# Kernel tuning notes

Hardware: AMD Instinct MI355X
Metric: run time of the kernel (lower is better)

Reference implementation:

```python
import jax, jax.numpy as jnp
import numpy as np


def setup_inputs() -> dict:
    key = jax.random.key(0)
    ks = jax.random.split(key, 6)
    B, C, H, W, K = 4, 64, 352, 1216, 3
    OC = K * K - 1  # 8 guide channels from convbn
    return {
        "feature": jax.random.normal(ks[0], (B, C, H, W), jnp.float32),
        "conv_w": jax.random.normal(ks[1], (OC, C, 3, 3), jnp.float32) * 0.05,
        "gamma": jax.random.uniform(ks[2], (OC,), jnp.float32, 0.5, 1.5),
        "beta": jax.random.normal(ks[3], (OC,), jnp.float32) * 0.1,
        "mean": jax.random.normal(ks[4], (OC,), jnp.float32) * 0.1,
        "var": jax.random.uniform(ks[5], (OC,), jnp.float32, 0.5, 1.5),
        "kernel_size": K,
    }


def reference(feature, conv_w, gamma, beta, mean, var, kernel_size):
    k = kernel_size
    eps = 1e-5
    # conv 3x3, stride 1, pad 1, no bias  -> [B, k*k-1, H, W]
    x = jax.lax.conv_general_dilated(
        feature, conv_w, window_strides=(1, 1), padding=((1, 1), (1, 1)),
        dimension_numbers=("NCHW", "OIHW", "NCHW"))
    c = lambda v: v[None, :, None, None]
    # BatchNorm2d in eval mode (running stats + affine)
    guide = (x - c(mean)) * (c(gamma) * jax.lax.rsqrt(c(var) + eps)) + c(beta)
    # L1-normalize across channels, middle weight = 1 - sum of the others
    gsum = jnp.sum(jnp.abs(guide), axis=1, keepdims=True)
    guide = guide / gsum
    guide_mid = 1.0 - jnp.sum(guide, axis=1, keepdims=True)
    mid = (k * k - 1) // 2
    # per-offset zero-pad each single channel into [H+k-1, W+k-1] canvas
    pads = []
    for t in range(k * k):  # fixed small loop over kernel offsets (k*k = 9)
        i, j = t // k, t % k  # top=i, bottom=k-1-i, left=j, right=k-1-j
        if t < mid:
            ch = guide[:, t:t + 1]
        elif t > mid:
            ch = guide[:, t - 1:t]
        else:
            ch = guide_mid
        pads.append(jnp.pad(ch, ((0, 0), (0, 0), (i, k - 1 - i), (j, k - 1 - j))))
    return jnp.concatenate(pads, axis=1)  # [B, k*k, H+k-1, W+k-1]
```

## Files before the change

kernel.cpp:

```cpp
#include <hip/hip_runtime.h>
#include <hip/hip_bf16.h>

#define BATCH 4
#define CIN 64
#define HH 352
#define WW 1216
#define OCH 8
#define OHH 354
#define OWW 1218
#define HW (HH * WW)

#define BH 16
#define BW 32
#define FR 18
#define FC 34
#define NPOS (FR * FC)
#define NTHR 256

typedef short bf16x8 __attribute__((ext_vector_type(8)));
typedef float f32x4  __attribute__((ext_vector_type(4)));

static __device__ __forceinline__ unsigned f2bf(float x) {
    unsigned u = __float_as_uint(x);
    return (u + 0x7FFFu + ((u >> 16) & 1u)) >> 16;
}

__global__ void repack_kernel(const float* __restrict__ conv_w,
                              const float* __restrict__ gamma,
                              const float* __restrict__ beta,
                              const float* __restrict__ mean,
                              const float* __restrict__ var,
                              unsigned short* __restrict__ wB,
                              float* __restrict__ bias)
{
    int tid = blockIdx.x * 256 + threadIdx.x;
    if (tid < 18 * 64) {
        int tc = tid >> 6;
        int lane = tid & 63;
        int tap = tc >> 1, cc = tc & 1;
        int oc = lane & 15, hi = lane >> 4;
        unsigned v[8];
#pragma unroll
        for (int j = 0; j < 8; ++j) {
            float w = 0.f;
            if (oc < 8) {
                int c = cc * 32 + hi * 8 + j;
                float scl = gamma[oc] * rsqrtf(var[oc] + 1e-5f);
                w = conv_w[((size_t)oc * CIN + c) * 9 + tap] * scl;
            }
            v[j] = f2bf(w);
        }
        uint4 pk;
        pk.x = v[0] | (v[1] << 16);
        pk.y = v[2] | (v[3] << 16);
        pk.z = v[4] | (v[5] << 16);
        pk.w = v[6] | (v[7] << 16);
        ((uint4*)wB)[tid] = pk;
    }
    if (tid < OCH) {
        float scl = gamma[tid] * rsqrtf(var[tid] + 1e-5f);
        bias[tid] = beta[tid] - mean[tid] * scl;
    }
}

__global__ void border_kernel(float* __restrict__ out)
{
    const int bt = blockIdx.x;
    const int t = bt % 9;
    const int i = t / 3, j = t % 3;
    float* pl = out + (size_t)bt * OHH * OWW;
    const int r0 = (i == 0) ? HH : 0;
    const int r1 = (i == 2) ? 1 : (OHH - 1);
    const int c0 = (j == 0) ? WW : 0;
    const int c1 = (j == 2) ? 1 : (OWW - 1);
    const int nrow = 2 * OWW;
    for (int idx = threadIdx.x; idx < 2 * OWW + 2 * OHH; idx += blockDim.x) {
        if (idx < nrow) {
            int r = (idx < OWW) ? r0 : r1;
            int c = (idx < OWW) ? idx : idx - OWW;
            pl[(size_t)r * OWW + c] = 0.f;
        } else {
            int k = idx - nrow;
            int c = (k < OHH) ? c0 : c1;
            int r = (k < OHH) ? k : k - OHH;
            pl[(size_t)r * OWW + c] = 0.f;
        }
    }
}

__global__ __launch_bounds__(NTHR, 2)
void conv_mfma(const float* __restrict__ feature,
               const unsigned short* __restrict__ wB,
               const float* __restrict__ bias,
               float* __restrict__ out)
{
    __shared__ uint4 sF[NPOS * 4];

    const int tid  = threadIdx.x;
    const int wave = tid >> 6;
    const int lane = tid & 63;
    const int oc   = lane & 15;
    const int hi   = lane >> 4;
    const int b  = blockIdx.z;
    const int h0 = blockIdx.y * BH;
    const int w0 = blockIdx.x * BW;

    const float* fb = feature + (size_t)b * CIN * HW;

    f32x4 acc[4][2];
#pragma unroll
    for (int rr = 0; rr < 4; ++rr)
#pragma unroll
        for (int cg = 0; cg < 2; ++cg) acc[rr][cg] = (f32x4)0.f;

#pragma unroll 1
    for (int cc = 0; cc < 2; ++cc) {
        if (cc) __syncthreads();
#pragma unroll 1
        for (int it = 0; it < 10; ++it) {
            int task = it * NTHR + tid;
            if (task < NPOS * 4) {
                int pos = task >> 2;
                int oct = task & 3;
                int fr = pos / FC;
                int fc = pos - fr * FC;
                int gh = h0 - 1 + fr, gw = w0 - 1 + fc;
                bool ok = ((unsigned)gh < (unsigned)HH) && ((unsigned)gw < (unsigned)WW);
                float v[8];
#pragma unroll
                for (int j = 0; j < 8; ++j) v[j] = 0.f;
                if (ok) {
                    const float* sp = fb + (size_t)(cc * 32 + oct * 8) * HW + gh * WW + gw;
#pragma unroll
                    for (int j = 0; j < 8; ++j) v[j] = sp[(size_t)j * HW];
                }
                uint4 pk;
                pk.x = f2bf(v[0]) | (f2bf(v[1]) << 16);
                pk.y = f2bf(v[2]) | (f2bf(v[3]) << 16);
                pk.z = f2bf(v[4]) | (f2bf(v[5]) << 16);
                pk.w = f2bf(v[6]) | (f2bf(v[7]) << 16);
                sF[pos * 4 + oct] = pk;
            }
        }
        bf16x8 bw[9];
#pragma unroll
        for (int t = 0; t < 9; ++t)
            bw[t] = ((const bf16x8*)wB)[(t * 2 + cc) * 64 + lane];
        __syncthreads();
#pragma unroll
        for (int t = 0; t < 9; ++t) {
            const int dh = t / 3, dw = t % 3;
#pragma unroll
            for (int rr = 0; rr < 4; ++rr) {
                const int fr = wave * 4 + rr + dh;
#pragma unroll
                for (int cg = 0; cg < 2; ++cg) {
                    const int fc = cg * 16 + oc + dw;
                    bf16x8 av = *reinterpret_cast<const bf16x8*>(&sF[(fr * FC + fc) * 4 + hi]);
                    acc[rr][cg] = __builtin_amdgcn_mfma_f32_16x16x32_bf16(av, bw[t], acc[rr][cg], 0, 0, 0);
                }
            }
        }
    }

    const float myb = (oc < 8) ? bias[oc] : 0.f;
    const int t = (oc < 8) ? ((oc < 4) ? oc : oc + 1) : 4;
    const bool dow = (oc <= 8);
    const int ii = t / 3, jj = t % 3;
    float* pl = out + ((size_t)(b * 9 + t) * OHH + ii) * OWW + jj;

#pragma unroll
    for (int rr = 0; rr < 4; ++rr) {
        const int h = h0 + wave * 4 + rr;
#pragma unroll
        for (int cg = 0; cg < 2; ++cg) {
#pragma unroll
            for (int reg = 0; reg < 4; ++reg) {
                float v = acc[rr][cg][reg] + myb;
                float av = fabsf(v);
                float sv = v;
                av += __shfl_xor(av, 1);  sv += __shfl_xor(sv, 1);
                av += __shfl_xor(av, 2);  sv += __shfl_xor(sv, 2);
                av += __shfl_xor(av, 4);  sv += __shfl_xor(sv, 4);
                av += __shfl_xor(av, 8);  sv += __shfl_xor(sv, 8);
                float inv = 1.0f / av;
                float val = (oc == 8) ? (1.0f - sv * inv) : (v * inv);
                if (dow) {
                    int w = w0 + cg * 16 + hi * 4 + reg;
                    pl[(size_t)h * OWW + w] = val;
                }
            }
        }
    }
}

extern "C" void kernel_launch(void* const* d_in, const int* in_sizes, int n_in,
                              void* d_out, int out_size, void* d_ws, size_t ws_size,
                              hipStream_t stream) {
    const float* feature = (const float*)d_in[0];
    const float* conv_w  = (const float*)d_in[1];
    const float* gamma   = (const float*)d_in[2];
    const float* beta    = (const float*)d_in[3];
    const float* mean    = (const float*)d_in[4];
    const float* var     = (const float*)d_in[5];
    float* out = (float*)d_out;
    unsigned short* wB = (unsigned short*)d_ws;
    float* bias = (float*)((char*)d_ws + 18432);

    border_kernel<<<BATCH * 9, 256, 0, stream>>>(out);
    repack_kernel<<<5, 256, 0, stream>>>(conv_w, gamma, beta, mean, var, wB, bias);

    dim3 grid(WW / BW, HH / BH, BATCH);
    conv_mfma<<<grid, NTHR, 0, stream>>>(feature, wB, bias, out);
}
```

Measured before the change: 251.8 us.

## Batch all feature loads before packing and swizzle LDS layout

Restructures the shared-memory fill so each thread issues all of its global loads up front, using clamped addresses and a validity mask instead of branches. It then packs to bf16 and writes to LDS. An XOR swizzle is applied to the LDS slot index on both write and read to reduce bank conflicts. The aim is more memory-level parallelism and cheaper LDS access, at the cost of many more live registers and possible occupancy loss or spills.

```diff
diff --git a/kernel.cpp b/kernel.cpp
--- a/kernel.cpp
+++ b/kernel.cpp
@@ -16,6 +16,8 @@
 #define FC 34
 #define NPOS (FR * FC)
 #define NTHR 256
+#define NTASK (NPOS * 4)
+#define NIT 10
 
 typedef short bf16x8 __attribute__((ext_vector_type(8)));
 typedef float f32x4  __attribute__((ext_vector_type(4)));
@@ -107,6 +109,9 @@
 
     const float* fb = feature + (size_t)b * CIN * HW;
 
+    const int soct = tid & 3;
+    const int p0   = tid >> 2;
+
     f32x4 acc[4][2];
 #pragma unroll
     for (int rr = 0; rr < 4; ++rr)
@@ -116,37 +121,44 @@
 #pragma unroll 1
     for (int cc = 0; cc < 2; ++cc) {
         if (cc) __syncthreads();
-#pragma unroll 1
-        for (int it = 0; it < 10; ++it) {
-            int task = it * NTHR + tid;
-            if (task < NPOS * 4) {
-                int pos = task >> 2;
-                int oct = task & 3;
-                int fr = pos / FC;
-                int fc = pos - fr * FC;
-                int gh = h0 - 1 + fr, gw = w0 - 1 + fc;
-                bool ok = ((unsigned)gh < (unsigned)HH) && ((unsigned)gw < (unsigned)WW);
-                float v[8];
-#pragma unroll
-                for (int j = 0; j < 8; ++j) v[j] = 0.f;
-                if (ok) {
-                    const float* sp = fb + (size_t)(cc * 32 + oct * 8) * HW + gh * WW + gw;
-#pragma unroll
-                    for (int j = 0; j < 8; ++j) v[j] = sp[(size_t)j * HW];
-                }
-                uint4 pk;
-                pk.x = f2bf(v[0]) | (f2bf(v[1]) << 16);
-                pk.y = f2bf(v[2]) | (f2bf(v[3]) << 16);
-                pk.z = f2bf(v[4]) | (f2bf(v[5]) << 16);
-                pk.w = f2bf(v[6]) | (f2bf(v[7]) << 16);
-                sF[pos * 4 + oct] = pk;
-            }
+
+        const float* chbase = fb + (size_t)(cc * 32 + soct * 8) * HW;
+        float v[NIT][8];
+        float msk[NIT];
+        int   cps[NIT];
+#pragma unroll
+        for (int it = 0; it < NIT; ++it) {
+            int pos = p0 + it * 64;
+            int cp = (pos < NPOS) ? pos : (NPOS - 1);
+            int fr = cp / FC;
+            int fc = cp - fr * FC;
+            int gh = h0 - 1 + fr, gw = w0 - 1 + fc;
+            bool ok = ((unsigned)gh < (unsigned)HH) && ((unsigned)gw < (unsigned)WW);
+            int sgh = min(max(gh, 0), HH - 1);
+            int sgw = min(max(gw, 0), WW - 1);
+            const float* sp = chbase + sgh * WW + sgw;
+#pragma unroll
+            for (int j = 0; j < 8; ++j) v[it][j] = sp[(size_t)j * HW];
+            msk[it] = ok ? 1.f : 0.f;
+            cps[it] = cp;
         }
         bf16x8 bw[9];
 #pragma unroll
         for (int t = 0; t < 9; ++t)
             bw[t] = ((const bf16x8*)wB)[(t * 2 + cc) * 64 + lane];
+#pragma unroll
+        for (int it = 0; it < NIT; ++it) {
+            float mk = msk[it];
+            uint4 pk;
+            pk.x = f2bf(v[it][0] * mk) | (f2bf(v[it][1] * mk) << 16);
+            pk.y = f2bf(v[it][2] * mk) | (f2bf(v[it][3] * mk) << 16);
+            pk.z = f2bf(v[it][4] * mk) | (f2bf(v[it][5] * mk) << 16);
+            pk.w = f2bf(v[it][6] * mk) | (f2bf(v[it][7] * mk) << 16);
+            int cp = cps[it];
+            sF[cp * 4 + (soct ^ ((cp >> 1) & 3))] = pk;
+        }
         __syncthreads();
+
 #pragma unroll
         for (int t = 0; t < 9; ++t) {
             const int dh = t / 3, dw = t % 3;
@@ -156,7 +168,8 @@
 #pragma unroll
                 for (int cg = 0; cg < 2; ++cg) {
                     const int fc = cg * 16 + oc + dw;
-                    bf16x8 av = *reinterpret_cast<const bf16x8*>(&sF[(fr * FC + fc) * 4 + hi]);
+                    const int pp = fr * FC + fc;
+                    bf16x8 av = *reinterpret_cast<const bf16x8*>(&sF[pp * 4 + (hi ^ ((pp >> 1) & 3))]);
                     acc[rr][cg] = __builtin_amdgcn_mfma_f32_16x16x32_bf16(av, bw[t], acc[rr][cg], 0, 0, 0);
                 }
             }
```

Measured after the change: 261.0 us. 1.04x slower.
